# Kernel tuning notes

Measured on AMD Instinct MI355X. Metric: run time of the kernel, lower is better.

## Reference

```python
import jax, jax.numpy as jnp
import numpy as np

B, S, D, H = 2, 2048, 1024, 16
HD = D // H


def _linear_params(key, scale):
    kw, kb = jax.random.split(key)
    W = jax.random.normal(kw, (D, D), dtype=jnp.float32) * scale
    b = jax.random.normal(kb, (D,), dtype=jnp.float32) * scale
    return W, b


def setup_inputs() -> dict:
    key = jax.random.key(0)
    keys = jax.random.split(key, 10)
    scale = 1.0 / np.sqrt(D)
    vis = jax.random.normal(keys[0], (B, S, D), dtype=jnp.float32)
    inf = jax.random.normal(keys[1], (B, S, D), dtype=jnp.float32)
    names = ["q_vis", "k_vis", "v_vis", "q_inf", "k_inf", "v_inf", "o_vis", "o_inf"]
    out = {"vis": vis, "inf": inf}
    for n, k in zip(names, keys[2:]):
        W, b = _linear_params(k, scale)
        out["W_" + n] = W
        out["b_" + n] = b
    return out


def _heads(x):
    # [B,S,D] -> [B,H,S,HD]
    return x.reshape(B, S, H, HD).transpose(0, 2, 1, 3)


def _merge(x):
    # [B,H,S,HD] -> [B,S,D]
    return x.transpose(0, 2, 1, 3).reshape(B, S, D)


def reference(vis, inf, W_q_vis, b_q_vis, W_k_vis, b_k_vis, W_v_vis, b_v_vis,
              W_q_inf, b_q_inf, W_k_inf, b_k_inf, W_v_inf, b_v_inf,
              W_o_vis, b_o_vis, W_o_inf, b_o_inf):
    Qv = _heads(vis @ W_q_vis + b_q_vis)
    Kv = _heads(vis @ W_k_vis + b_k_vis)
    Vv = _heads(vis @ W_v_vis + b_v_vis)
    Qi = _heads(inf @ W_q_inf + b_q_inf)
    Ki = _heads(inf @ W_k_inf + b_k_inf)
    Vi = _heads(inf @ W_v_inf + b_v_inf)
    scale = 1.0 / jnp.sqrt(jnp.float32(HD))
    # vis queries attend over inf keys/values
    scores_vi = jnp.einsum("bhqd,bhkd->bhqk", Qv, Ki) * scale
    attn_inf = jax.nn.softmax(scores_vi, axis=-1)
    out_inf = jnp.einsum("bhqk,bhkd->bhqd", attn_inf, Vi)
    # inf queries attend over vis keys/values
    scores_iv = jnp.einsum("bhqd,bhkd->bhqk", Qi, Kv) * scale
    attn_vis = jax.nn.softmax(scores_iv, axis=-1)
    out_vis = jnp.einsum("bhqk,bhkd->bhqd", attn_vis, Vv)
    out_vis = _merge(out_vis) @ W_o_vis + b_o_vis
    out_inf = _merge(out_inf) @ W_o_inf + b_o_inf
    return (out_vis, out_inf)
```

## Files before the change

### kernel.cpp

```cpp
#include <hip/hip_runtime.h>
#include <hip/hip_bf16.h>

#define DEV __device__ __forceinline__

typedef __attribute__((ext_vector_type(4))) float f32x4;
typedef __attribute__((ext_vector_type(16))) float f32x16;
typedef __attribute__((ext_vector_type(8))) __bf16 bf16x8;
typedef __attribute__((ext_vector_type(8))) unsigned short ushort8;
typedef __attribute__((ext_vector_type(4))) unsigned int uint32x4;

static constexpr int BATCH = 2, SEQ = 2048, DM = 1024, NH = 16, HDIM = 64;
static constexpr size_t XSZ = (size_t)BATCH * SEQ * DM;

DEV unsigned short f2bf(float f) {
  union { float f; unsigned int u; } v; v.f = f;
  unsigned int r = (v.u + 0x7fffu + ((v.u >> 16) & 1u)) >> 16;
  return (unsigned short)r;
}

DEV bf16x8 ld8(const unsigned short* p) {
  return __builtin_bit_cast(bf16x8, *(const ushort8*)p);
}

DEV f32x4 mfma16(bf16x8 a, bf16x8 b, f32x4 c) {
  return __builtin_amdgcn_mfma_f32_16x16x32_bf16(a, b, c, 0, 0, 0);
}
DEV f32x16 mfma32(bf16x8 a, bf16x8 b, f32x16 c) {
  return __builtin_amdgcn_mfma_f32_32x32x16_bf16(a, b, c, 0, 0, 0);
}

DEV unsigned cvtpk(float lo, float hi) {
  unsigned r;
  asm("v_cvt_pk_bf16_f32 %0, %1, %2" : "=v"(r) : "v"(lo), "v"(hi));
  return r;
}
DEV void plswap(unsigned& a, unsigned& b) {
  asm("v_permlane32_swap_b32 %0, %1" : "+v"(a), "+v"(b));
}

DEV void gll16(const unsigned short* g, unsigned short* l) {
  __builtin_amdgcn_global_load_lds(
      (__attribute__((address_space(1))) void*)(unsigned short*)g,
      (__attribute__((address_space(3))) void*)l, 16, 0, 0);
}

__global__ __launch_bounds__(256)
void k_convert_x(const float* __restrict__ vis, const float* __restrict__ inff,
                 unsigned short* __restrict__ out) {
  const float* src = blockIdx.z ? inff : vis;
  unsigned short* dst = out + (size_t)blockIdx.z * XSZ;
  const size_t i = ((size_t)blockIdx.x * 256 + threadIdx.x) * 8;
  const float4 a = *(const float4*)(src + i);
  const float4 b = *(const float4*)(src + i + 4);
  ushort8 v;
  v[0] = f2bf(a.x); v[1] = f2bf(a.y); v[2] = f2bf(a.z); v[3] = f2bf(a.w);
  v[4] = f2bf(b.x); v[5] = f2bf(b.y); v[6] = f2bf(b.z); v[7] = f2bf(b.w);
  *(ushort8*)(dst + i) = v;
}

struct WPtrs { const float* w[8]; };

__global__ __launch_bounds__(256)
void k_convert_w(WPtrs p, unsigned short* __restrict__ wt) {
  const float* W = p.w[blockIdx.z];
  unsigned short* Wt = wt + (size_t)blockIdx.z * (1024 * 1024);
  const int k0 = blockIdx.y * 64, n0 = blockIdx.x * 64;
  __shared__ unsigned short t[64][68];
  const int tx = threadIdx.x & 15, ty = threadIdx.x >> 4;
#pragma unroll
  for (int i = 0; i < 4; ++i) {
    const int kr = ty * 4 + i;
    const float4 v = *(const float4*)(W + (size_t)(k0 + kr) * 1024 + n0 + tx * 4);
    t[kr][tx * 4 + 0] = f2bf(v.x); t[kr][tx * 4 + 1] = f2bf(v.y);
    t[kr][tx * 4 + 2] = f2bf(v.z); t[kr][tx * 4 + 3] = f2bf(v.w);
  }
  __syncthreads();
#pragma unroll
  for (int i = 0; i < 4; ++i) {
    const int nr = ty * 4 + i;
    ushort4 o;
    o.x = t[tx * 4 + 0][nr]; o.y = t[tx * 4 + 1][nr];
    o.z = t[tx * 4 + 2][nr]; o.w = t[tx * 4 + 3][nr];
    *(ushort4*)(Wt + (size_t)(n0 + nr) * 1024 + k0 + tx * 4) = o;
  }
}

struct GemmJob { const unsigned short* A; const unsigned short* W;
                 const float* bias; void* out; float scale; };
struct GemmJobs { GemmJob j[6]; };

template<int MODE>
__global__ __launch_bounds__(256)
void k_gemm(GemmJobs jobs) {
  const GemmJob jb = jobs.j[blockIdx.z];
  const int lane = threadIdx.x & 63, w = threadIdx.x >> 6;
  const int wr = w >> 1, wc = w & 1;
  const int r = lane & 15, g = lane >> 4;
  const int bm = blockIdx.y * 128, bn = blockIdx.x * 128;

  __shared__ __align__(16) unsigned short As[128 * 64];
  __shared__ __align__(16) unsigned short Bs[128 * 64];

  const int srow = lane >> 3;
  const int schunk = (lane & 7) ^ srow;
  const unsigned short* Ag = jb.A + (size_t)(bm + w * 32 + srow) * DM + schunk * 8;
  const unsigned short* Bg = jb.W + (size_t)(bn + w * 32 + srow) * DM + schunk * 8;

  f32x4 acc[4][4] = {};

  for (int kt = 0; kt < DM; kt += 64) {
#pragma unroll
    for (int j = 0; j < 4; ++j) {
      gll16(Ag + kt + j * 8 * DM, As + (w * 4 + j) * 512);
      gll16(Bg + kt + j * 8 * DM, Bs + (w * 4 + j) * 512);
    }
    __syncthreads();
#pragma unroll
    for (int kk = 0; kk < 2; ++kk) {
      bf16x8 a[4], b[4];
#pragma unroll
      for (int m = 0; m < 4; ++m) {
        const int row = wr * 64 + m * 16 + r;
        const int pos = (kk * 4 + g) ^ (row & 7);
        a[m] = ld8(As + row * 64 + pos * 8);
      }
#pragma unroll
      for (int n = 0; n < 4; ++n) {
        const int row = wc * 64 + n * 16 + r;
        const int pos = (kk * 4 + g) ^ (row & 7);
        b[n] = ld8(Bs + row * 64 + pos * 8);
      }
#pragma unroll
      for (int m = 0; m < 4; ++m)
#pragma unroll
        for (int n = 0; n < 4; ++n)
          acc[m][n] = mfma16(a[m], b[n], acc[m][n]);
    }
    __syncthreads();
  }

  if (MODE == 0) {
    unsigned short* O = (unsigned short*)jb.out;
#pragma unroll
    for (int n = 0; n < 4; ++n) {
      const int nc = bn + wc * 64 + n * 16 + r;
      const float bv = jb.bias[nc];
      const int h = nc >> 6, hd = nc & 63;
#pragma unroll
      for (int m = 0; m < 4; ++m)
#pragma unroll
        for (int i = 0; i < 4; ++i) {
          const int mr = bm + wr * 64 + m * 16 + g * 4 + i;
          const int bb = mr >> 11, s = mr & 2047;
          O[((size_t)(bb * NH + h) * SEQ + s) * HDIM + hd] =
              f2bf((acc[m][n][i] + bv) * jb.scale);
        }
    }
  } else {
    float* O = (float*)jb.out;
#pragma unroll
    for (int n = 0; n < 4; ++n) {
      const int nc = bn + wc * 64 + n * 16 + r;
      const float bv = jb.bias[nc];
#pragma unroll
      for (int m = 0; m < 4; ++m)
#pragma unroll
        for (int i = 0; i < 4; ++i) {
          const int mr = bm + wr * 64 + m * 16 + g * 4 + i;
          O[(size_t)mr * DM + nc] = acc[m][n][i] + bv;
        }
    }
  }
}

__global__ __launch_bounds__(256)
void k_transpose_v(const unsigned short* __restrict__ Vv, const unsigned short* __restrict__ Vi,
                   unsigned short* __restrict__ Vvt, unsigned short* __restrict__ Vit) {
  const unsigned short* src = blockIdx.z ? Vi : Vv;
  unsigned short* dst = blockIdx.z ? Vit : Vvt;
  const int bh = blockIdx.y;
  const int s0 = blockIdx.x * 64;
  __shared__ unsigned short t[64][68];
  const int tx = threadIdx.x & 15, ty = threadIdx.x >> 4;
#pragma unroll
  for (int i = 0; i < 4; ++i) {
    const int sr = ty * 4 + i;
    const ushort4 v = *(const ushort4*)(src + ((size_t)bh * SEQ + s0 + sr) * HDIM + tx * 4);
    t[sr][tx * 4 + 0] = v.x; t[sr][tx * 4 + 1] = v.y;
    t[sr][tx * 4 + 2] = v.z; t[sr][tx * 4 + 3] = v.w;
  }
  __syncthreads();
#pragma unroll
  for (int i = 0; i < 4; ++i) {
    const int dr = ty * 4 + i;
    ushort4 o;
    o.x = t[tx * 4 + 0][dr]; o.y = t[tx * 4 + 1][dr];
    o.z = t[tx * 4 + 2][dr]; o.w = t[tx * 4 + 3][dr];
    *(ushort4*)(dst + ((size_t)bh * HDIM + dr) * SEQ + s0 + tx * 4) = o;
  }
}

struct AttnJob { const unsigned short* Q; const unsigned short* K;
                 const unsigned short* Vt; unsigned short* O; };
struct AttnJobs { AttnJob j[2]; };

__global__ __launch_bounds__(256)
void k_attn(AttnJobs jobs) {
  const AttnJob jb = jobs.j[blockIdx.z];
  const int bh = blockIdx.y;
  const int lane = threadIdx.x & 63, w = threadIdx.x >> 6;
  const int q5 = lane & 31, hi = lane >> 5;
  const int qrow = blockIdx.x * 128 + w * 32 + q5;

  const unsigned short* Qp = jb.Q + (size_t)bh * SEQ * HDIM;
  const unsigned short* Kp = jb.K + (size_t)bh * SEQ * HDIM;
  const unsigned short* Vp = jb.Vt + (size_t)bh * HDIM * SEQ;

  __shared__ __align__(16) unsigned short Ks[2][64 * 64];
  __shared__ __align__(16) unsigned short Vs[2][64 * 64];

  bf16x8 qf[4];
#pragma unroll
  for (int c = 0; c < 4; ++c)
    qf[c] = ld8(Qp + (size_t)qrow * HDIM + c * 16 + hi * 8);

  const int srow = lane >> 3;
  const int sslot = lane & 7;

  auto stage = [&](int buf, int kv0) {
#pragma unroll
    for (int j = 0; j < 2; ++j) {
      const int row = j * 32 + w * 8 + srow;
      const int u = sslot ^ (row & 7);
      gll16(Kp + (size_t)(kv0 + row) * HDIM + u * 8, Ks[buf] + (j * 32 + w * 8) * 64);
      gll16(Vp + (size_t)row * SEQ + kv0 + u * 8,    Vs[buf] + (j * 32 + w * 8) * 64);
    }
  };

  f32x16 o0 = {}, o1 = {};
  float mrow = -1e30f, lrow = 0.f;
  const int swz = q5 & 7;

  stage(0, 0);
  __syncthreads();

  for (int t = 0; t < SEQ / 64; ++t) {
    const int cur = t & 1;
    if (t + 1 < SEQ / 64) stage(cur ^ 1, (t + 1) * 64);

    f32x16 s0 = {}, s1 = {};
    __builtin_amdgcn_s_setprio(1);
#pragma unroll
    for (int c = 0; c < 4; ++c) {
      const int sl = ((2 * c + hi) ^ swz) * 8;
      s0 = mfma32(ld8(Ks[cur] + q5 * 64 + sl), qf[c], s0);
      s1 = mfma32(ld8(Ks[cur] + (32 + q5) * 64 + sl), qf[c], s1);
    }
    __builtin_amdgcn_s_setprio(0);

    float tm[8];
#pragma unroll
    for (int r = 0; r < 8; ++r)
      tm[r] = fmaxf(fmaxf(s0[r], s0[r + 8]), fmaxf(s1[r], s1[r + 8]));
    float mx = fmaxf(fmaxf(fmaxf(tm[0], tm[1]), fmaxf(tm[2], tm[3])),
                     fmaxf(fmaxf(tm[4], tm[5]), fmaxf(tm[6], tm[7])));
    mx = fmaxf(mx, __shfl_xor(mx, 32, 64));

    if (!__all(mx <= mrow + 8.f)) {
      const float mn = fmaxf(mx, mrow);
      const float al = __expf(mrow - mn);
      mrow = mn;
      lrow *= al;
#pragma unroll
      for (int r = 0; r < 16; ++r) { o0[r] *= al; o1[r] *= al; }
    }

    float ps = 0.f, ps2 = 0.f;
#pragma unroll
    for (int r = 0; r < 16; ++r) {
      s0[r] = __expf(s0[r] - mrow); ps += s0[r];
      s1[r] = __expf(s1[r] - mrow); ps2 += s1[r];
    }
    lrow += ps + ps2;

    unsigned pk0[8], pk1[8];
#pragma unroll
    for (int ww = 0; ww < 8; ++ww) {
      pk0[ww] = cvtpk(s0[2 * ww], s0[2 * ww + 1]);
      pk1[ww] = cvtpk(s1[2 * ww], s1[2 * ww + 1]);
    }

    __builtin_amdgcn_s_setprio(1);
#pragma unroll
    for (int c = 0; c < 4; ++c) {
      const int wb = 4 * (c & 1);
      unsigned a0 = (c < 2) ? pk0[wb + 0] : pk1[wb + 0];
      unsigned a1 = (c < 2) ? pk0[wb + 1] : pk1[wb + 1];
      unsigned b0 = (c < 2) ? pk0[wb + 2] : pk1[wb + 2];
      unsigned b1 = (c < 2) ? pk0[wb + 3] : pk1[wb + 3];
      plswap(a0, b0);
      plswap(a1, b1);
      uint32x4 fw = {a0, a1, b0, b1};
      const bf16x8 pf = __builtin_bit_cast(bf16x8, fw);
      const int sl = ((2 * c + hi) ^ swz) * 8;
      o0 = mfma32(ld8(Vs[cur] + q5 * 64 + sl), pf, o0);
      o1 = mfma32(ld8(Vs[cur] + (32 + q5) * 64 + sl), pf, o1);
    }
    __builtin_amdgcn_s_setprio(0);

    __syncthreads();
  }

  const float ltot = lrow + __shfl_xor(lrow, 32, 64);
  const float inv = 1.f / ltot;
  const int bb = bh >> 4, h = bh & 15;
  unsigned short* Ob = jb.O + ((size_t)bb * SEQ + qrow) * DM + h * HDIM;

  auto storeO = [&](const f32x16 oo, int dbase) {
#pragma unroll
    for (int g4 = 0; g4 < 4; ++g4) {
      ushort4 pv;
      pv.x = f2bf(oo[4 * g4 + 0] * inv);
      pv.y = f2bf(oo[4 * g4 + 1] * inv);
      pv.z = f2bf(oo[4 * g4 + 2] * inv);
      pv.w = f2bf(oo[4 * g4 + 3] * inv);
      *(ushort4*)(Ob + dbase + 8 * g4 + 4 * hi) = pv;
    }
  };
  storeO(o0, 0);
  storeO(o1, 32);
}

extern "C" void kernel_launch(void* const* d_in, const int* in_sizes, int n_in,
                              void* d_out, int out_size, void* d_ws, size_t ws_size,
                              hipStream_t stream) {
  const float* vis = (const float*)d_in[0];
  const float* inff = (const float*)d_in[1];

  unsigned short* xbf  = (unsigned short*)d_ws;
  unsigned short* wt   = xbf + 2 * XSZ;
  unsigned short* Qv   = wt + (size_t)8 * 1024 * 1024;
  unsigned short* Kv   = Qv + XSZ;
  unsigned short* Vv   = Kv + XSZ;
  unsigned short* Qi   = Vv + XSZ;
  unsigned short* Ki   = Qi + XSZ;
  unsigned short* Vi   = Ki + XSZ;
  unsigned short* Vvt  = Vi + XSZ;
  unsigned short* Vit  = Vvt + XSZ;
  unsigned short* atA  = Vit + XSZ;
  unsigned short* atB  = atA + XSZ;

  k_convert_x<<<dim3(2048, 1, 2), 256, 0, stream>>>(vis, inff, xbf);

  WPtrs wp;
  wp.w[0] = (const float*)d_in[2];  wp.w[1] = (const float*)d_in[4];
  wp.w[2] = (const float*)d_in[6];  wp.w[3] = (const float*)d_in[8];
  wp.w[4] = (const float*)d_in[10]; wp.w[5] = (const float*)d_in[12];
  wp.w[6] = (const float*)d_in[14]; wp.w[7] = (const float*)d_in[16];
  k_convert_w<<<dim3(16, 16, 8), 256, 0, stream>>>(wp, wt);

  const size_t WSZ = (size_t)1024 * 1024;
  const float sc = 0.125f;
  GemmJobs pj;
  pj.j[0] = { xbf,       wt + 0 * WSZ, (const float*)d_in[3],  (void*)Qv, sc };
  pj.j[1] = { xbf,       wt + 1 * WSZ, (const float*)d_in[5],  (void*)Kv, 1.f };
  pj.j[2] = { xbf,       wt + 2 * WSZ, (const float*)d_in[7],  (void*)Vv, 1.f };
  pj.j[3] = { xbf + XSZ, wt + 3 * WSZ, (const float*)d_in[9],  (void*)Qi, sc };
  pj.j[4] = { xbf + XSZ, wt + 4 * WSZ, (const float*)d_in[11], (void*)Ki, 1.f };
  pj.j[5] = { xbf + XSZ, wt + 5 * WSZ, (const float*)d_in[13], (void*)Vi, 1.f };
  k_gemm<0><<<dim3(8, 32, 6), 256, 0, stream>>>(pj);

  k_transpose_v<<<dim3(32, 32, 2), 256, 0, stream>>>(Vv, Vi, Vvt, Vit);

  AttnJobs aj;
  aj.j[0] = { Qv, Ki, Vit, atA };
  aj.j[1] = { Qi, Kv, Vvt, atB };
  k_attn<<<dim3(16, 32, 2), 256, 0, stream>>>(aj);

  GemmJobs oj;
  oj.j[0] = { atB, wt + 6 * WSZ, (const float*)d_in[15], d_out, 1.f };
  oj.j[1] = { atA, wt + 7 * WSZ, (const float*)d_in[17], (void*)((float*)d_out + XSZ), 1.f };
  for (int z = 2; z < 6; ++z) oj.j[z] = oj.j[0];
  k_gemm<1><<<dim3(8, 32, 2), 256, 0, stream>>>(oj);
}
```

Baseline: 353.2 us.

## Fuse V transpose into projection GEMM, use exp2 softmax, remap blocks

The V projection GEMM now writes V directly in head-dim-major layout through a new epilogue mode, which removes the separate transpose kernel and its round trip through memory. The attention softmax folds log2(e) into the Q scale and calls the native exp2. It raises the rescale threshold and computes the row sum with an extra MFMA against a ones vector in place of scalar adds. Both the GEMM and attention grids remap block indices so neighbouring blocks share tiles in cache. The GEMM mode moves from a template parameter to a runtime field, which adds a branch, and the extra MFMA per step adds matrix work.

```diff
diff --git a/kernel.cpp b/kernel.cpp
--- a/kernel.cpp
+++ b/kernel.cpp
@@ -86,17 +86,20 @@
 }
 
 struct GemmJob { const unsigned short* A; const unsigned short* W;
-                 const float* bias; void* out; float scale; };
+                 const float* bias; void* out; float scale; int mode; };
 struct GemmJobs { GemmJob j[6]; };
 
-template<int MODE>
 __global__ __launch_bounds__(256)
 void k_gemm(GemmJobs jobs) {
   const GemmJob jb = jobs.j[blockIdx.z];
   const int lane = threadIdx.x & 63, w = threadIdx.x >> 6;
   const int wr = w >> 1, wc = w & 1;
   const int r = lane & 15, g = lane >> 4;
-  const int bm = blockIdx.y * 128, bn = blockIdx.x * 128;
+
+  const int nid = blockIdx.x + (blockIdx.y << 3);
+  const int bxs = nid >> 5;
+  const int bys = ((nid & 7) << 2) + ((nid >> 3) & 3);
+  const int bm = bys * 128, bn = bxs * 128;
 
   __shared__ __align__(16) unsigned short As[128 * 64];
   __shared__ __align__(16) unsigned short Bs[128 * 64];
@@ -139,7 +142,7 @@
     __syncthreads();
   }
 
-  if (MODE == 0) {
+  if (jb.mode == 0) {
     unsigned short* O = (unsigned short*)jb.out;
 #pragma unroll
     for (int n = 0; n < 4; ++n) {
@@ -156,6 +159,25 @@
               f2bf((acc[m][n][i] + bv) * jb.scale);
         }
     }
+  } else if (jb.mode == 2) {
+    unsigned short* O = (unsigned short*)jb.out;
+#pragma unroll
+    for (int n = 0; n < 4; ++n) {
+      const int nc = bn + wc * 64 + n * 16 + r;
+      const float bv = jb.bias[nc];
+      const int h = nc >> 6, hd = nc & 63;
+#pragma unroll
+      for (int m = 0; m < 4; ++m) {
+        const int mr = bm + wr * 64 + m * 16 + g * 4;
+        const int bb = mr >> 11, s = mr & 2047;
+        ushort4 pv;
+        pv.x = f2bf(acc[m][n][0] + bv);
+        pv.y = f2bf(acc[m][n][1] + bv);
+        pv.z = f2bf(acc[m][n][2] + bv);
+        pv.w = f2bf(acc[m][n][3] + bv);
+        *(ushort4*)(O + ((size_t)(bb * NH + h) * HDIM + hd) * SEQ + s) = pv;
+      }
+    }
   } else {
     float* O = (float*)jb.out;
 #pragma unroll
@@ -173,33 +195,6 @@
   }
 }
 
-__global__ __launch_bounds__(256)
-void k_transpose_v(const unsigned short* __restrict__ Vv, const unsigned short* __restrict__ Vi,
-                   unsigned short* __restrict__ Vvt, unsigned short* __restrict__ Vit) {
-  const unsigned short* src = blockIdx.z ? Vi : Vv;
-  unsigned short* dst = blockIdx.z ? Vit : Vvt;
-  const int bh = blockIdx.y;
-  const int s0 = blockIdx.x * 64;
-  __shared__ unsigned short t[64][68];
-  const int tx = threadIdx.x & 15, ty = threadIdx.x >> 4;
-#pragma unroll
-  for (int i = 0; i < 4; ++i) {
-    const int sr = ty * 4 + i;
-    const ushort4 v = *(const ushort4*)(src + ((size_t)bh * SEQ + s0 + sr) * HDIM + tx * 4);
-    t[sr][tx * 4 + 0] = v.x; t[sr][tx * 4 + 1] = v.y;
-    t[sr][tx * 4 + 2] = v.z; t[sr][tx * 4 + 3] = v.w;
-  }
-  __syncthreads();
-#pragma unroll
-  for (int i = 0; i < 4; ++i) {
-    const int dr = ty * 4 + i;
-    ushort4 o;
-    o.x = t[tx * 4 + 0][dr]; o.y = t[tx * 4 + 1][dr];
-    o.z = t[tx * 4 + 2][dr]; o.w = t[tx * 4 + 3][dr];
-    *(ushort4*)(dst + ((size_t)bh * HDIM + dr) * SEQ + s0 + tx * 4) = o;
-  }
-}
-
 struct AttnJob { const unsigned short* Q; const unsigned short* K;
                  const unsigned short* Vt; unsigned short* O; };
 struct AttnJobs { AttnJob j[2]; };
@@ -207,10 +202,12 @@
 __global__ __launch_bounds__(256)
 void k_attn(AttnJobs jobs) {
   const AttnJob jb = jobs.j[blockIdx.z];
-  const int bh = blockIdx.y;
+  const int nid = blockIdx.x + (blockIdx.y << 4);
+  const int bx = nid >> 5;
+  const int bh = ((nid & 7) << 2) + ((nid >> 3) & 3);
   const int lane = threadIdx.x & 63, w = threadIdx.x >> 6;
   const int q5 = lane & 31, hi = lane >> 5;
-  const int qrow = blockIdx.x * 128 + w * 32 + q5;
+  const int qrow = bx * 128 + w * 32 + q5;
 
   const unsigned short* Qp = jb.Q + (size_t)bh * SEQ * HDIM;
   const unsigned short* Kp = jb.K + (size_t)bh * SEQ * HDIM;
@@ -223,6 +220,11 @@
 #pragma unroll
   for (int c = 0; c < 4; ++c)
     qf[c] = ld8(Qp + (size_t)qrow * HDIM + c * 16 + hi * 8);
+
+  ushort8 ov; 
+#pragma unroll
+  for (int i = 0; i < 8; ++i) ov[i] = 0x3f80;
+  const bf16x8 onesb = __builtin_bit_cast(bf16x8, ov);
 
   const int srow = lane >> 3;
   const int sslot = lane & 7;
@@ -237,8 +239,8 @@
     }
   };
 
-  f32x16 o0 = {}, o1 = {};
-  float mrow = -1e30f, lrow = 0.f;
+  f32x16 o0 = {}, o1 = {}, lsum = {};
+  float mrow = -1e30f;
   const int swz = q5 & 7;
 
   stage(0, 0);
@@ -262,26 +264,24 @@
 #pragma unroll
     for (int r = 0; r < 8; ++r)
       tm[r] = fmaxf(fmaxf(s0[r], s0[r + 8]), fmaxf(s1[r], s1[r + 8]));
-    float mx = fmaxf(fmaxf(fmaxf(tm[0], tm[1]), fmaxf(tm[2], tm[3])),
-                     fmaxf(fmaxf(tm[4], tm[5]), fmaxf(tm[6], tm[7])));
+    float mx = fmaxf(fmaxf(fmaxf(tm[0], tm[1]), tm[2]),
+                     fmaxf(fmaxf(tm[3], tm[4]), fmaxf(fmaxf(tm[5], tm[6]), tm[7])));
     mx = fmaxf(mx, __shfl_xor(mx, 32, 64));
 
-    if (!__all(mx <= mrow + 8.f)) {
+    if (!__all(mx <= mrow + 11.5416f)) {
       const float mn = fmaxf(mx, mrow);
-      const float al = __expf(mrow - mn);
+      const float al = __builtin_amdgcn_exp2f(mrow - mn);
       mrow = mn;
-      lrow *= al;
+      lsum[0] *= al;
 #pragma unroll
       for (int r = 0; r < 16; ++r) { o0[r] *= al; o1[r] *= al; }
     }
 
-    float ps = 0.f, ps2 = 0.f;
 #pragma unroll
     for (int r = 0; r < 16; ++r) {
-      s0[r] = __expf(s0[r] - mrow); ps += s0[r];
-      s1[r] = __expf(s1[r] - mrow); ps2 += s1[r];
-    }
-    lrow += ps + ps2;
+      s0[r] = __builtin_amdgcn_exp2f(s0[r] - mrow);
+      s1[r] = __builtin_amdgcn_exp2f(s1[r] - mrow);
+    }
 
     unsigned pk0[8], pk1[8];
 #pragma unroll
@@ -305,14 +305,14 @@
       const int sl = ((2 * c + hi) ^ swz) * 8;
       o0 = mfma32(ld8(Vs[cur] + q5 * 64 + sl), pf, o0);
       o1 = mfma32(ld8(Vs[cur] + (32 + q5) * 64 + sl), pf, o1);
+      lsum = mfma32(onesb, pf, lsum);
     }
     __builtin_amdgcn_s_setprio(0);
 
     __syncthreads();
   }
 
-  const float ltot = lrow + __shfl_xor(lrow, 32, 64);
-  const float inv = 1.f / ltot;
+  const float inv = 1.f / lsum[0];
   const int bb = bh >> 4, h = bh & 15;
   unsigned short* Ob = jb.O + ((size_t)bb * SEQ + qrow) * DM + h * HDIM;
 
@@ -360,17 +360,15 @@
   k_convert_w<<<dim3(16, 16, 8), 256, 0, stream>>>(wp, wt);
 
   const size_t WSZ = (size_t)1024 * 1024;
-  const float sc = 0.125f;
+  const float qsc = 0.18033688011f;
   GemmJobs pj;
-  pj.j[0] = { xbf,       wt + 0 * WSZ, (const float*)d_in[3],  (void*)Qv, sc };
-  pj.j[1] = { xbf,       wt + 1 * WSZ, (const float*)d_in[5],  (void*)Kv, 1.f };
-  pj.j[2] = { xbf,       wt + 2 * WSZ, (const float*)d_in[7],  (void*)Vv, 1.f };
-  pj.j[3] = { xbf + XSZ, wt + 3 * WSZ, (const float*)d_in[9],  (void*)Qi, sc };
-  pj.j[4] = { xbf + XSZ, wt + 4 * WSZ, (const float*)d_in[11], (void*)Ki, 1.f };
-  pj.j[5] = { xbf + XSZ, wt + 5 * WSZ, (const float*)d_in[13], (void*)Vi, 1.f };
-  k_gemm<0><<<dim3(8, 32, 6), 256, 0, stream>>>(pj);
-
-  k_transpose_v<<<dim3(32, 32, 2), 256, 0, stream>>>(Vv, Vi, Vvt, Vit);
+  pj.j[0] = { xbf,       wt + 0 * WSZ, (const float*)d_in[3],  (void*)Qv,  qsc, 0 };
+  pj.j[1] = { xbf,       wt + 1 * WSZ, (const float*)d_in[5],  (void*)Kv,  1.f, 0 };
+  pj.j[2] = { xbf,       wt + 2 * WSZ, (const float*)d_in[7],  (void*)Vvt, 1.f, 2 };
+  pj.j[3] = { xbf + XSZ, wt + 3 * WSZ, (const float*)d_in[9],  (void*)Qi,  qsc, 0 };
+  pj.j[4] = { xbf + XSZ, wt + 4 * WSZ, (const float*)d_in[11], (void*)Ki,  1.f, 0 };
+  pj.j[5] = { xbf + XSZ, wt + 5 * WSZ, (const float*)d_in[13], (void*)Vit, 1.f, 2 };
+  k_gemm<<<dim3(8, 32, 6), 256, 0, stream>>>(pj);
 
   AttnJobs aj;
   aj.j[0] = { Qv, Ki, Vit, atA };
@@ -378,8 +376,8 @@
   k_attn<<<dim3(16, 32, 2), 256, 0, stream>>>(aj);
 
   GemmJobs oj;
-  oj.j[0] = { atB, wt + 6 * WSZ, (const float*)d_in[15], d_out, 1.f };
-  oj.j[1] = { atA, wt + 7 * WSZ, (const float*)d_in[17], (void*)((float*)d_out + XSZ), 1.f };
+  oj.j[0] = { atB, wt + 6 * WSZ, (const float*)d_in[15], d_out, 1.f, 1 };
+  oj.j[1] = { atA, wt + 7 * WSZ, (const float*)d_in[17], (void*)((float*)d_out + XSZ), 1.f, 1 };
   for (int z = 2; z < 6; ++z) oj.j[z] = oj.j[0];
-  k_gemm<1><<<dim3(8, 32, 2), 256, 0, stream>>>(oj);
-}
+  k_gemm<<<dim3(8, 32, 2), 256, 0, stream>>>(oj);
+}
```

Measured after the change: 324.7 us. -8.1%, faster.
